# Kernel tuning notes

Hardware: AMD Instinct MI355X
Metric: run time of the kernel (lower is better)

## Reference

```python
import jax, jax.numpy as jnp
import numpy as np

N, M, Z_DIM = 32768, 8192, 64


def setup_inputs() -> dict:
    key = jax.random.key(0)
    kz, ke = jax.random.split(key)
    z = jax.random.normal(kz, (N, Z_DIM), dtype=jnp.float32)
    # torch: e = rand(M, z_dim) * 2 - 1  -> uniform in [-1, 1)
    e = jax.random.uniform(ke, (M, Z_DIM), dtype=jnp.float32, minval=-1.0, maxval=1.0)
    return {"z": z, "e": e}


def reference(z, e):
    # data['z'] = tanh(z)
    zt = jnp.tanh(z)                                   # (N, Z)
    # pairwise squared distance via Gram expansion:
    # ||a - b||^2 = ||a||^2 + ||b||^2 - 2 a.b  (same math as the
    # broadcasted sum((a-b)**2) without the (N, M, Z) intermediate)
    zn = jnp.sum(zt * zt, axis=1)                      # (N,)
    en = jnp.sum(e * e, axis=1)                        # (M,)
    distance = zn[:, None] + en[None, :] - 2.0 * (zt @ e.T)   # (N, M)
    # min over the batch dim N for each sample e, then mean over M
    loss = jnp.mean(jnp.min(distance, axis=0))
    return loss
```

## Files before the change

kernel.cpp:

```cpp
#include <hip/hip_runtime.h>
#include <hip/hip_bf16.h>
#include <math.h>

#define NN 32768
#define MM 8192
#define ZD 64
#define WAVES 4
#define MW 64
#define MBLK (WAVES * MW)
#define NMB (MM / MBLK)
#define NCHUNKS 32
#define CHUNK (NN / NCHUNKS)
#define NROWS 128
#define NITER (CHUNK / NROWS)
#define SCALE 4294967296.0

typedef __attribute__((ext_vector_type(8))) short bf16x8;
typedef __attribute__((ext_vector_type(4))) float f32x4;

__device__ inline unsigned short f2bf(float f) {
  unsigned u = __float_as_uint(f);
  return (unsigned short)((u + 0x7fffu + ((u >> 16) & 1u)) >> 16);
}
__device__ inline float bf2f(unsigned short h) {
  return __uint_as_float(((unsigned)h) << 16);
}

__global__ __launch_bounds__(256) void prep(
    const float* __restrict__ z, const float* __restrict__ e,
    unsigned short* __restrict__ zb, float* __restrict__ zn,
    unsigned short* __restrict__ eb, float* __restrict__ en,
    unsigned* __restrict__ dmin, unsigned long long* __restrict__ acc,
    unsigned* __restrict__ cnt) {
  const int q = threadIdx.x & 7;
  if (blockIdx.x < NN / 32) {
    const int row = blockIdx.x * 32 + (threadIdx.x >> 3);
    const size_t base = (size_t)row * ZD + q * 8;
    float4 v0 = *reinterpret_cast<const float4*>(&z[base]);
    float4 v1 = *reinterpret_cast<const float4*>(&z[base + 4]);
    float in[8] = {v0.x, v0.y, v0.z, v0.w, v1.x, v1.y, v1.z, v1.w};
    unsigned short b[8];
    float s = 0.f;
#pragma unroll
    for (int i = 0; i < 8; ++i) {
      b[i] = f2bf(tanhf(in[i]));
      float r = bf2f(b[i]);
      s += r * r;
    }
    *reinterpret_cast<bf16x8*>(&zb[base]) = *reinterpret_cast<bf16x8*>(b);
    s += __shfl_xor(s, 1, 64);
    s += __shfl_xor(s, 2, 64);
    s += __shfl_xor(s, 4, 64);
    if (q == 0) zn[row] = s;
  } else {
    const int row = (blockIdx.x - NN / 32) * 32 + (threadIdx.x >> 3);
    const size_t base = (size_t)row * ZD + q * 8;
    float4 v0 = *reinterpret_cast<const float4*>(&e[base]);
    float4 v1 = *reinterpret_cast<const float4*>(&e[base + 4]);
    float in[8] = {v0.x, v0.y, v0.z, v0.w, v1.x, v1.y, v1.z, v1.w};
    unsigned short b[8];
    float s = 0.f;
#pragma unroll
    for (int i = 0; i < 8; ++i) {
      unsigned short qb = f2bf(in[i]);
      float r = bf2f(qb);
      s += r * r;
      b[i] = f2bf(-2.f * r);
    }
    *reinterpret_cast<bf16x8*>(&eb[base]) = *reinterpret_cast<bf16x8*>(b);
    s += __shfl_xor(s, 1, 64);
    s += __shfl_xor(s, 2, 64);
    s += __shfl_xor(s, 4, 64);
    if (q == 0) {
      en[row] = s;
      dmin[row] = 0xFFFFFFFFu;
    }
    if (blockIdx.x == NN / 32 && threadIdx.x == 0) {
      *acc = 0ULL;
      *cnt = 0u;
    }
  }
}

__global__ __launch_bounds__(256, 4) void min_dist(
    const unsigned short* __restrict__ zb, const unsigned short* __restrict__ eb,
    const float* __restrict__ zn, unsigned* __restrict__ dmin) {
  __shared__ __align__(128) unsigned short zlds[2][NROWS * ZD];
  const int wg = ((blockIdx.x & 7) << 7) + (blockIdx.x >> 3);
  const int mb = wg & (NMB - 1);
  const int cb = wg >> 5;
  const int lane = threadIdx.x & 63;
  const int wv = threadIdx.x >> 6;
  const int lr = lane & 15;
  const int lg = lane >> 4;
  const int m0 = mb * MBLK + wv * MW;
  const int nb0 = cb * CHUNK;

  const int srow = lane >> 3;
  const int sslot = (lane & 7) ^ srow;
  const char* zsrc = (const char*)zb + (size_t)nb0 * 128 +
                     (wv * 32 + srow) * 128 + (sslot << 4);
  char* ldst0 = (char*)&zlds[0][0] + wv * 4096;
  char* ldst1 = (char*)&zlds[1][0] + wv * 4096;

  bf16x8 bfr[4][2];
#pragma unroll
  for (int t = 0; t < 4; ++t)
#pragma unroll
    for (int h = 0; h < 2; ++h)
      bfr[t][h] = *reinterpret_cast<const bf16x8*>(
          &eb[(size_t)(m0 + t * 16 + lr) * ZD + h * 32 + lg * 8]);

  float minv[4] = {3.4e38f, 3.4e38f, 3.4e38f, 3.4e38f};

  auto stage = [&](char* dst, const char* src) {
#pragma unroll
    for (int j = 0; j < 4; ++j)
      __builtin_amdgcn_global_load_lds(
          (const __attribute__((address_space(1))) unsigned int*)(src + j * 1024),
          (__attribute__((address_space(3))) unsigned int*)(dst + j * 1024),
          16, 0, 0);
  };

  const float* znp = zn + nb0;
  const int x0 = (lg * 16) ^ ((lr & 7) << 4);

  stage(ldst0, zsrc);
  zsrc += NROWS * 128;
  __syncthreads();

  for (int it = 0; it < NITER; ++it) {
    const char* lbase = (it & 1) ? (const char*)&zlds[1][0] : (const char*)&zlds[0][0];
    if (it + 1 < NITER) {
      stage((it & 1) ? ldst0 : ldst1, zsrc);
      zsrc += NROWS * 128;
    }
#pragma unroll
    for (int s = 0; s < NROWS / 16; ++s) {
      const int rb = (s * 16 + lr) * 128;
      bf16x8 a0 = *reinterpret_cast<const bf16x8*>(lbase + rb + x0);
      bf16x8 a1 = *reinterpret_cast<const bf16x8*>(lbase + rb + (x0 ^ 64));
      f32x4 znv = *reinterpret_cast<const f32x4*>(znp + s * 16 + lg * 4);
#pragma unroll
      for (int t = 0; t < 4; ++t) {
        f32x4 acc = __builtin_amdgcn_mfma_f32_16x16x32_bf16(a0, bfr[t][0], znv, 0, 0, 0);
        acc = __builtin_amdgcn_mfma_f32_16x16x32_bf16(a1, bfr[t][1], acc, 0, 0, 0);
        float x = fminf(fminf(acc[0], acc[1]), acc[2]);
        minv[t] = fminf(fminf(x, acc[3]), minv[t]);
      }
    }
    znp += NROWS;
    __syncthreads();
  }

#pragma unroll
  for (int t = 0; t < 4; ++t) {
    float v = minv[t];
    v = fminf(v, __shfl_xor(v, 16, 64));
    v = fminf(v, __shfl_xor(v, 32, 64));
    if (lg == 0) {
      unsigned bits = __float_as_uint(v);
      unsigned key = (bits & 0x80000000u) ? ~bits : (bits | 0x80000000u);
      atomicMin(&dmin[m0 + t * 16 + lr], key);
    }
  }
}

__global__ __launch_bounds__(256) void finalize(const unsigned* __restrict__ dmin,
                                                const float* __restrict__ en,
                                                unsigned long long* __restrict__ acc,
                                                unsigned* __restrict__ cnt,
                                                float* __restrict__ out) {
  const int m = blockIdx.x * 256 + threadIdx.x;
  unsigned key = dmin[m];
  unsigned bits = (key & 0x80000000u) ? (key & 0x7FFFFFFFu) : ~key;
  float mv = __uint_as_float(bits);
  double s = (double)(mv + en[m]);
  __shared__ double sred[256];
  sred[threadIdx.x] = s;
  __syncthreads();
  for (int off = 128; off > 0; off >>= 1) {
    if ((int)threadIdx.x < off) sred[threadIdx.x] += sred[threadIdx.x + off];
    __syncthreads();
  }
  if (threadIdx.x == 0) {
    unsigned long long iv = (unsigned long long)(sred[0] * SCALE + 0.5);
    atomicAdd(acc, iv);
    __threadfence();
    unsigned d = atomicAdd(cnt, 1u);
    if (d == MM / 256 - 1) {
      __threadfence();
      unsigned long long tot = atomicAdd(acc, 0ULL);
      out[0] = (float)((double)tot / SCALE / (double)MM);
    }
  }
}

extern "C" void kernel_launch(void* const* d_in, const int* in_sizes, int n_in,
                              void* d_out, int out_size, void* d_ws, size_t ws_size,
                              hipStream_t stream) {
  const float* z = (const float*)d_in[0];
  const float* e = (const float*)d_in[1];
  float* out = (float*)d_out;

  unsigned short* zb = (unsigned short*)d_ws;
  unsigned short* eb = zb + (size_t)NN * ZD;
  float* zn = (float*)(eb + (size_t)MM * ZD);
  float* en = zn + NN;
  unsigned* dmin = (unsigned*)(en + MM);
  unsigned long long* acc = (unsigned long long*)(dmin + MM);
  unsigned* cnt = (unsigned*)(acc + 1);

  prep<<<(NN + MM) / 32, 256, 0, stream>>>(z, e, zb, zn, eb, en, dmin, acc, cnt);
  min_dist<<<NMB * NCHUNKS, 256, 0, stream>>>(zb, eb, zn, dmin);
  finalize<<<MM / 256, 256, 0, stream>>>(dmin, en, acc, cnt, out);
}
```

Before: 46.60 us.

## Widen per-wave M tile and fuse final reduction into min_dist via last-block

Each wave now covers 128 columns of e (8 MFMA tiles) instead of 64, so every z tile staged into LDS is reused across twice as many e columns. N is split into 64 chunks so the grid stays at 1024 blocks. The separate finalize kernel is removed: the last block to finish, found with an atomic counter, reduces dmin+en and writes the mean, which saves a kernel launch. The cost is more registers per wave (16 B-fragments, 8 mins), which may hurt occupancy, plus a serial 8192-element reduction in a single block.

```diff
diff --git a/kernel.cpp b/kernel.cpp
--- a/kernel.cpp
+++ b/kernel.cpp
@@ -6,14 +6,14 @@
 #define MM 8192
 #define ZD 64
 #define WAVES 4
-#define MW 64
+#define MW 128
 #define MBLK (WAVES * MW)
 #define NMB (MM / MBLK)
-#define NCHUNKS 32
+#define NCHUNKS 64
 #define CHUNK (NN / NCHUNKS)
 #define NROWS 128
 #define NITER (CHUNK / NROWS)
-#define SCALE 4294967296.0
+#define GRID (NMB * NCHUNKS)
 
 typedef __attribute__((ext_vector_type(8))) short bf16x8;
 typedef __attribute__((ext_vector_type(4))) float f32x4;
@@ -30,8 +30,7 @@
     const float* __restrict__ z, const float* __restrict__ e,
     unsigned short* __restrict__ zb, float* __restrict__ zn,
     unsigned short* __restrict__ eb, float* __restrict__ en,
-    unsigned* __restrict__ dmin, unsigned long long* __restrict__ acc,
-    unsigned* __restrict__ cnt) {
+    unsigned* __restrict__ dmin, unsigned* __restrict__ cnt) {
   const int q = threadIdx.x & 7;
   if (blockIdx.x < NN / 32) {
     const int row = blockIdx.x * 32 + (threadIdx.x >> 3);
@@ -75,20 +74,19 @@
       en[row] = s;
       dmin[row] = 0xFFFFFFFFu;
     }
-    if (blockIdx.x == NN / 32 && threadIdx.x == 0) {
-      *acc = 0ULL;
-      *cnt = 0u;
-    }
+    if (blockIdx.x == NN / 32 && threadIdx.x == 0) *cnt = 0u;
   }
 }
 
 __global__ __launch_bounds__(256, 4) void min_dist(
     const unsigned short* __restrict__ zb, const unsigned short* __restrict__ eb,
-    const float* __restrict__ zn, unsigned* __restrict__ dmin) {
+    const float* __restrict__ zn, const float* __restrict__ en,
+    unsigned* __restrict__ dmin, unsigned* __restrict__ cnt,
+    float* __restrict__ out) {
   __shared__ __align__(128) unsigned short zlds[2][NROWS * ZD];
   const int wg = ((blockIdx.x & 7) << 7) + (blockIdx.x >> 3);
   const int mb = wg & (NMB - 1);
-  const int cb = wg >> 5;
+  const int cb = wg >> 4;
   const int lane = threadIdx.x & 63;
   const int wv = threadIdx.x >> 6;
   const int lr = lane & 15;
@@ -103,15 +101,16 @@
   char* ldst0 = (char*)&zlds[0][0] + wv * 4096;
   char* ldst1 = (char*)&zlds[1][0] + wv * 4096;
 
-  bf16x8 bfr[4][2];
-#pragma unroll
-  for (int t = 0; t < 4; ++t)
+  bf16x8 bfr[8][2];
+#pragma unroll
+  for (int t = 0; t < 8; ++t)
 #pragma unroll
     for (int h = 0; h < 2; ++h)
       bfr[t][h] = *reinterpret_cast<const bf16x8*>(
           &eb[(size_t)(m0 + t * 16 + lr) * ZD + h * 32 + lg * 8]);
 
-  float minv[4] = {3.4e38f, 3.4e38f, 3.4e38f, 3.4e38f};
+  float minv[8] = {3.4e38f, 3.4e38f, 3.4e38f, 3.4e38f,
+                   3.4e38f, 3.4e38f, 3.4e38f, 3.4e38f};
 
   auto stage = [&](char* dst, const char* src) {
 #pragma unroll
@@ -142,7 +141,7 @@
       bf16x8 a1 = *reinterpret_cast<const bf16x8*>(lbase + rb + (x0 ^ 64));
       f32x4 znv = *reinterpret_cast<const f32x4*>(znp + s * 16 + lg * 4);
 #pragma unroll
-      for (int t = 0; t < 4; ++t) {
+      for (int t = 0; t < 8; ++t) {
         f32x4 acc = __builtin_amdgcn_mfma_f32_16x16x32_bf16(a0, bfr[t][0], znv, 0, 0, 0);
         acc = __builtin_amdgcn_mfma_f32_16x16x32_bf16(a1, bfr[t][1], acc, 0, 0, 0);
         float x = fminf(fminf(acc[0], acc[1]), acc[2]);
@@ -154,7 +153,7 @@
   }
 
 #pragma unroll
-  for (int t = 0; t < 4; ++t) {
+  for (int t = 0; t < 8; ++t) {
     float v = minv[t];
     v = fminf(v, __shfl_xor(v, 16, 64));
     v = fminf(v, __shfl_xor(v, 32, 64));
@@ -164,18 +163,20 @@
       atomicMin(&dmin[m0 + t * 16 + lr], key);
     }
   }
-}
-
-__global__ __launch_bounds__(256) void finalize(const unsigned* __restrict__ dmin,
-                                                const float* __restrict__ en,
-                                                unsigned long long* __restrict__ acc,
-                                                unsigned* __restrict__ cnt,
-                                                float* __restrict__ out) {
-  const int m = blockIdx.x * 256 + threadIdx.x;
-  unsigned key = dmin[m];
-  unsigned bits = (key & 0x80000000u) ? (key & 0x7FFFFFFFu) : ~key;
-  float mv = __uint_as_float(bits);
-  double s = (double)(mv + en[m]);
+
+  __threadfence();
+  __syncthreads();
+  __shared__ bool isLast;
+  if (threadIdx.x == 0) isLast = (atomicAdd(cnt, 1u) == GRID - 1);
+  __syncthreads();
+  if (!isLast) return;
+  __threadfence();
+  double s = 0.0;
+  for (int m = threadIdx.x; m < MM; m += 256) {
+    unsigned key = dmin[m];
+    unsigned bits = (key & 0x80000000u) ? (key & 0x7FFFFFFFu) : ~key;
+    s += (double)(__uint_as_float(bits) + en[m]);
+  }
   __shared__ double sred[256];
   sred[threadIdx.x] = s;
   __syncthreads();
@@ -183,17 +184,7 @@
     if ((int)threadIdx.x < off) sred[threadIdx.x] += sred[threadIdx.x + off];
     __syncthreads();
   }
-  if (threadIdx.x == 0) {
-    unsigned long long iv = (unsigned long long)(sred[0] * SCALE + 0.5);
-    atomicAdd(acc, iv);
-    __threadfence();
-    unsigned d = atomicAdd(cnt, 1u);
-    if (d == MM / 256 - 1) {
-      __threadfence();
-      unsigned long long tot = atomicAdd(acc, 0ULL);
-      out[0] = (float)((double)tot / SCALE / (double)MM);
-    }
-  }
+  if (threadIdx.x == 0) out[0] = (float)(sred[0] / (double)MM);
 }
 
 extern "C" void kernel_launch(void* const* d_in, const int* in_sizes, int n_in,
@@ -208,10 +199,8 @@
   float* zn = (float*)(eb + (size_t)MM * ZD);
   float* en = zn + NN;
   unsigned* dmin = (unsigned*)(en + MM);
-  unsigned long long* acc = (unsigned long long*)(dmin + MM);
-  unsigned* cnt = (unsigned*)(acc + 1);
-
-  prep<<<(NN + MM) / 32, 256, 0, stream>>>(z, e, zb, zn, eb, en, dmin, acc, cnt);
-  min_dist<<<NMB * NCHUNKS, 256, 0, stream>>>(zb, eb, zn, dmin);
-  finalize<<<MM / 256, 256, 0, stream>>>(dmin, en, acc, cnt, out);
-}
+  unsigned* cnt = dmin + MM;
+
+  prep<<<(NN + MM) / 32, 256, 0, stream>>>(z, e, zb, zn, eb, en, dmin, cnt);
+  min_dist<<<GRID, 256, 0, stream>>>(zb, eb, zn, en, dmin, cnt, out);
+}
```

Measured after the change: 132.5 us. 2.84x slower.
